# Kernel optimization log

Measured on AMD Instinct MI355X. Metric: run time of the kernel, lower is better.

Reference implementation:

```python
import jax, jax.numpy as jnp
import numpy as np

B, S, D = 16, 512, 13 * 768  # batch, pad_size, (num_layers+1)*hidden
H1, H2 = 1000, 40


def setup_inputs() -> dict:
    key = jax.random.key(0)
    k = jax.random.split(key, 5)
    hidden_states = jax.random.normal(k[0], (B, S, D), dtype=jnp.float32)
    # monotonically increasing subword start indices; 0 == padding slot
    token_starts = jnp.sort(jax.random.randint(k[1], (B, S), 0, S), axis=1).astype(jnp.int64)
    W1 = jax.random.normal(k[2], (D, H1), dtype=jnp.float32) * 0.02
    b1 = jnp.zeros((H1,), dtype=jnp.float32)
    W2 = jax.random.normal(k[3], (H1, H2), dtype=jnp.float32) * 0.02
    b2 = jnp.zeros((H2,), dtype=jnp.float32)
    W3 = jax.random.normal(k[4], (H2, 1), dtype=jnp.float32) * 0.02
    b3 = jnp.zeros((1,), dtype=jnp.float32)
    return {"hidden_states": hidden_states, "token_starts": token_starts,
            "W1": W1, "b1": b1, "W2": W2, "b2": b2, "W3": W3, "b3": b3}


def reference(hidden_states, token_starts, W1, b1, W2, b2, W3, b3):
    # MLP head over concatenated per-layer hidden states: [B,S,D] -> [B,S]
    h = jax.nn.relu(jnp.einsum('bsd,dh->bsh', hidden_states, W1) + b1)
    h = jax.nn.relu(jnp.einsum('bsh,hk->bsk', h, W2) + b2)
    pred_logits = jax.nn.sigmoid(jnp.einsum('bsk,ko->bso', h, W3) + b3)[..., 0]  # [B,S]
    # ragged gather: pred_labels[b,w] = pred_logits[b, token_starts[b,w]] if start != 0 else 0
    gathered = jnp.take_along_axis(pred_logits, token_starts, axis=1)
    pred_labels = jnp.where(token_starts != 0, gathered, jnp.float32(0.0))
    return pred_labels
```

## Files before the change

### kernel.cpp

```cpp
#include <hip/hip_runtime.h>

typedef __bf16 bf16x8 __attribute__((ext_vector_type(8)));
typedef float  f32x4  __attribute__((ext_vector_type(4)));

#define D_DIM 9984
#define H1P   1024
#define M_DIM 8192

__device__ __forceinline__ void gld_lds16(const void* g, void* l) {
  __builtin_amdgcn_global_load_lds((__attribute__((address_space(1))) void*)(g),
                                   (__attribute__((address_space(3))) void*)(l),
                                   16, 0, 0);
}

__global__ __launch_bounds__(256) void k_cvt_a(const float* __restrict__ A,
                                               __bf16* __restrict__ Ab) {
  const size_t t = (size_t)blockIdx.x * 256 + threadIdx.x;
  const float4* p = (const float4*)A + t * 2;
  const float4 a = p[0], b = p[1];
  bf16x8 o;
  o[0] = (__bf16)a.x; o[1] = (__bf16)a.y; o[2] = (__bf16)a.z; o[3] = (__bf16)a.w;
  o[4] = (__bf16)b.x; o[5] = (__bf16)b.y; o[6] = (__bf16)b.z; o[7] = (__bf16)b.w;
  *(bf16x8*)(Ab + t * 8) = o;
}

__global__ __launch_bounds__(256) void k_transpose_w1(const float* __restrict__ W1,
                                                      __bf16* __restrict__ W1T) {
  __shared__ float tile[32][33];
  const int bk = blockIdx.x, bn = blockIdx.y;
  const int tx = threadIdx.x, ty = threadIdx.y;
#pragma unroll
  for (int i = 0; i < 4; ++i) {
    const int kk = bk * 32 + ty + i * 8;
    const int nn = bn * 32 + tx;
    tile[ty + i * 8][tx] = (nn < 1000) ? W1[(size_t)kk * 1000 + nn] : 0.f;
  }
  __syncthreads();
#pragma unroll
  for (int i = 0; i < 4; ++i) {
    const int nn = bn * 32 + ty + i * 8;
    const int kk = bk * 32 + tx;
    W1T[(size_t)nn * D_DIM + kk] = (__bf16)tile[tx][ty + i * 8];
  }
}

__global__ void k_prep_w2(const float* __restrict__ W2, __bf16* __restrict__ W2T) {
  const int idx = blockIdx.x * 256 + threadIdx.x;
  const int j = idx >> 10, k = idx & 1023;
  const float v = (j < 40 && k < 1000) ? W2[k * 40 + j] : 0.f;
  W2T[idx] = (__bf16)v;
}

__global__ __launch_bounds__(256) void k_gemm1b(const __bf16* __restrict__ A,
                                                const __bf16* __restrict__ BT,
                                                const float* __restrict__ b1,
                                                __bf16* __restrict__ C) {
  __shared__ __bf16 As[128 * 32];
  __shared__ __bf16 Bs[128 * 32];
  const int tid  = threadIdx.x;
  const int lane = tid & 63;
  const int wid  = tid >> 6;
  const int tm = blockIdx.x, tn = blockIdx.y;
  const int wm = wid & 1, wn = wid >> 1;

  const int c0 = wid * 2, c1 = c0 + 1;
  const int lr = lane >> 2;
  const int lc = (lane & 3) * 8;
  const __bf16* ag0 = A  + (size_t)(tm * 128 + c0 * 16 + lr) * D_DIM + lc;
  const __bf16* ag1 = A  + (size_t)(tm * 128 + c1 * 16 + lr) * D_DIM + lc;
  const __bf16* bg0 = BT + (size_t)(tn * 128 + c0 * 16 + lr) * D_DIM + lc;
  const __bf16* bg1 = BT + (size_t)(tn * 128 + c1 * 16 + lr) * D_DIM + lc;
  __bf16* al0 = &As[c0 * 16 * 32];
  __bf16* al1 = &As[c1 * 16 * 32];
  __bf16* bl0 = &Bs[c0 * 16 * 32];
  __bf16* bl1 = &Bs[c1 * 16 * 32];

  const int fr = lane & 15;
  const int kq = (lane >> 4) * 8;
  f32x4 acc[4][4] = {};

  for (int i = 0; i < 312; ++i) {
    const size_t k0 = (size_t)i * 32;
    __syncthreads();
    gld_lds16(ag0 + k0, al0);
    gld_lds16(ag1 + k0, al1);
    gld_lds16(bg0 + k0, bl0);
    gld_lds16(bg1 + k0, bl1);
    __syncthreads();
    bf16x8 af[4], bf[4];
#pragma unroll
    for (int mi = 0; mi < 4; ++mi)
      af[mi] = *(const bf16x8*)&As[(wm * 64 + mi * 16 + fr) * 32 + kq];
#pragma unroll
    for (int ni = 0; ni < 4; ++ni)
      bf[ni] = *(const bf16x8*)&Bs[(wn * 64 + ni * 16 + fr) * 32 + kq];
#pragma unroll
    for (int mi = 0; mi < 4; ++mi)
#pragma unroll
      for (int ni = 0; ni < 4; ++ni)
        acc[mi][ni] = __builtin_amdgcn_mfma_f32_16x16x32_bf16(af[mi], bf[ni], acc[mi][ni], 0, 0, 0);
  }

  const int row0 = tm * 128 + wm * 64 + ((lane >> 4) << 2);
  const int col0 = tn * 128 + wn * 64 + fr;
#pragma unroll
  for (int ni = 0; ni < 4; ++ni) {
    const int col = col0 + ni * 16;
    const float bias = (col < 1000) ? b1[col] : 0.f;
#pragma unroll
    for (int mi = 0; mi < 4; ++mi)
#pragma unroll
      for (int r = 0; r < 4; ++r) {
        const float v = acc[mi][ni][r] + bias;
        C[(size_t)(row0 + mi * 16 + r) * H1P + col] = (__bf16)fmaxf(v, 0.f);
      }
  }
}

__global__ __launch_bounds__(256) void k_gemm1(const float* __restrict__ A,
                                               const __bf16* __restrict__ BT,
                                               const float* __restrict__ b1,
                                               __bf16* __restrict__ C) {
  __shared__ __bf16 As[128 * 32];
  __shared__ __bf16 Bs[128 * 32];
  const int tid  = threadIdx.x;
  const int lane = tid & 63;
  const int wid  = tid >> 6;
  const int tm = blockIdx.x, tn = blockIdx.y;
  const int wm = wid & 1, wn = wid >> 1;

  const int arow = tid >> 1;
  const int acol = (tid & 1) * 16;
  const float* ag = A + (size_t)(tm * 128 + arow) * D_DIM + acol;
  __bf16* asw = &As[arow * 32 + acol];

  const int c0 = wid * 2, c1 = wid * 2 + 1;
  const __bf16* bg0 = BT + (size_t)(tn * 128 + c0 * 16 + (lane >> 2)) * D_DIM + (lane & 3) * 8;
  const __bf16* bg1 = BT + (size_t)(tn * 128 + c1 * 16 + (lane >> 2)) * D_DIM + (lane & 3) * 8;
  __bf16* bl0 = &Bs[c0 * 16 * 32];
  __bf16* bl1 = &Bs[c1 * 16 * 32];

  const int fr = lane & 15;
  const int kq = (lane >> 4) * 8;
  f32x4 acc[4][4] = {};

  float4 pa[4];
  {
    const float4* ap = (const float4*)ag;
    pa[0] = ap[0]; pa[1] = ap[1]; pa[2] = ap[2]; pa[3] = ap[3];
  }
  for (int i = 0; i < 312; ++i) {
    const int k0 = i * 32;
    __syncthreads();
    {
      const float* pf = (const float*)pa;
      bf16x8 w0, w1;
#pragma unroll
      for (int j = 0; j < 8; ++j) { w0[j] = (__bf16)pf[j]; w1[j] = (__bf16)pf[j + 8]; }
      *(bf16x8*)asw       = w0;
      *(bf16x8*)(asw + 8) = w1;
    }
    gld_lds16(bg0 + k0, bl0);
    gld_lds16(bg1 + k0, bl1);
    __syncthreads();
    if (i != 311) {
      const float4* ap = (const float4*)(ag + k0 + 32);
      pa[0] = ap[0]; pa[1] = ap[1]; pa[2] = ap[2]; pa[3] = ap[3];
    }
    bf16x8 af[4], bf[4];
#pragma unroll
    for (int mi = 0; mi < 4; ++mi)
      af[mi] = *(const bf16x8*)&As[(wm * 64 + mi * 16 + fr) * 32 + kq];
#pragma unroll
    for (int ni = 0; ni < 4; ++ni)
      bf[ni] = *(const bf16x8*)&Bs[(wn * 64 + ni * 16 + fr) * 32 + kq];
#pragma unroll
    for (int mi = 0; mi < 4; ++mi)
#pragma unroll
      for (int ni = 0; ni < 4; ++ni)
        acc[mi][ni] = __builtin_amdgcn_mfma_f32_16x16x32_bf16(af[mi], bf[ni], acc[mi][ni], 0, 0, 0);
  }
  const int row0 = tm * 128 + wm * 64 + ((lane >> 4) << 2);
  const int col0 = tn * 128 + wn * 64 + fr;
#pragma unroll
  for (int ni = 0; ni < 4; ++ni) {
    const int col = col0 + ni * 16;
    const float bias = (col < 1000) ? b1[col] : 0.f;
#pragma unroll
    for (int mi = 0; mi < 4; ++mi)
#pragma unroll
      for (int r = 0; r < 4; ++r) {
        const float v = acc[mi][ni][r] + bias;
        C[(size_t)(row0 + mi * 16 + r) * H1P + col] = (__bf16)fmaxf(v, 0.f);
      }
  }
}

__global__ __launch_bounds__(256) void k_gemm2l(const __bf16* __restrict__ h1,
                                                const __bf16* __restrict__ W2T,
                                                const float* __restrict__ b2,
                                                const float* __restrict__ W3,
                                                const float* __restrict__ b3,
                                                float* __restrict__ lg) {
  __shared__ __bf16 As[64 * 32];
  __shared__ __bf16 Bs[64 * 32];
  const int tid  = threadIdx.x;
  const int lane = tid & 63;
  const int wid  = tid >> 6;
  const int bm   = blockIdx.x;

  const __bf16* ag = h1  + (size_t)(bm * 64 + wid * 16 + (lane >> 2)) * H1P + (lane & 3) * 8;
  const __bf16* bg = W2T + (size_t)(wid * 16 + (lane >> 2)) * H1P + (lane & 3) * 8;
  __bf16* al = &As[wid * 16 * 32];
  __bf16* bl = &Bs[wid * 16 * 32];

  const int fr = lane & 15;
  const int kq = (lane >> 4) * 8;
  f32x4 acc[4] = {};

  for (int i = 0; i < 32; ++i) {
    const int k0 = i * 32;
    __syncthreads();
    gld_lds16(ag + k0, al);
    gld_lds16(bg + k0, bl);
    __syncthreads();
    const bf16x8 a = *(const bf16x8*)&As[(wid * 16 + fr) * 32 + kq];
#pragma unroll
    for (int ni = 0; ni < 4; ++ni) {
      const bf16x8 b = *(const bf16x8*)&Bs[(ni * 16 + fr) * 32 + kq];
      acc[ni] = __builtin_amdgcn_mfma_f32_16x16x32_bf16(a, b, acc[ni], 0, 0, 0);
    }
  }
  float s[4] = {0.f, 0.f, 0.f, 0.f};
#pragma unroll
  for (int ni = 0; ni < 4; ++ni) {
    const int j = ni * 16 + fr;
    if (j < 40) {
      const float w3 = W3[j], bias = b2[j];
#pragma unroll
      for (int r = 0; r < 4; ++r)
        s[r] += fmaxf(acc[ni][r] + bias, 0.f) * w3;
    }
  }
#pragma unroll
  for (int off = 1; off < 16; off <<= 1)
#pragma unroll
    for (int r = 0; r < 4; ++r)
      s[r] += __shfl_xor(s[r], off, 16);
  if (fr == 0) {
    const int m0 = bm * 64 + wid * 16 + ((lane >> 4) << 2);
    const float b3v = b3[0];
#pragma unroll
    for (int r = 0; r < 4; ++r)
      lg[m0 + r] = 1.f / (1.f + __expf(-(s[r] + b3v)));
  }
}

__global__ void k_gather(const int* __restrict__ ts, const float* __restrict__ lg,
                         float* __restrict__ out) {
  const int t = blockIdx.x * 256 + threadIdx.x;
  const int b = t >> 9;
  const int s = ts[t];
  out[t] = (s > 0 && s < 512) ? lg[(b << 9) + s] : 0.f;
}

extern "C" void kernel_launch(void* const* d_in, const int* in_sizes, int n_in,
                              void* d_out, int out_size, void* d_ws, size_t ws_size,
                              hipStream_t stream) {
  const float* hs = (const float*)d_in[0];
  const int*   ts = (const int*)d_in[1];
  const float* W1 = (const float*)d_in[2];
  const float* b1 = (const float*)d_in[3];
  const float* W2 = (const float*)d_in[4];
  const float* b2 = (const float*)d_in[5];
  const float* W3 = (const float*)d_in[6];
  const float* b3 = (const float*)d_in[7];
  float* out = (float*)d_out;
  char* ws = (char*)d_ws;

  const size_t ABF = 163577856;
  const size_t NEED = ABF + 20447232 + 16777216 + 131072 + 32768;

  if (ws_size >= NEED) {
    __bf16* Ab  = (__bf16*)(ws);
    __bf16* W1T = (__bf16*)(ws + ABF);
    __bf16* h1  = (__bf16*)(ws + ABF + 20447232);
    __bf16* W2T = (__bf16*)(ws + ABF + 20447232 + 16777216);
    float*  lg  = (float*) (ws + ABF + 20447232 + 16777216 + 131072);

    k_cvt_a<<<39936, 256, 0, stream>>>(hs, Ab);
    k_transpose_w1<<<dim3(312, 32), dim3(32, 8), 0, stream>>>(W1, W1T);
    k_prep_w2<<<256, 256, 0, stream>>>(W2, W2T);
    k_gemm1b<<<dim3(64, 8), 256, 0, stream>>>(Ab, W1T, b1, h1);
    k_gemm2l<<<128, 256, 0, stream>>>(h1, W2T, b2, W3, b3, lg);
    k_gather<<<32, 256, 0, stream>>>(ts, lg, out);
  } else {
    __bf16* W1T = (__bf16*)(ws);
    __bf16* h1  = (__bf16*)(ws + 20447232);
    __bf16* W2T = (__bf16*)(ws + 20447232 + 16777216);
    float*  lg  = (float*) (ws + 20447232 + 16777216 + 131072);

    k_transpose_w1<<<dim3(312, 32), dim3(32, 8), 0, stream>>>(W1, W1T);
    k_prep_w2<<<256, 256, 0, stream>>>(W2, W2T);
    k_gemm1<<<dim3(64, 8), 256, 0, stream>>>(hs, W1T, b1, h1);
    k_gemm2l<<<128, 256, 0, stream>>>(h1, W2T, b2, W3, b3, lg);
    k_gather<<<32, 256, 0, stream>>>(ts, lg, out);
  }
}
```

Baseline: 724.6 us.

## Fuse prep kernels and add 4-stage async LDS pipeline to GEMM1

Merges the activation conversion, W1 transpose and W2 prep into one launch, cutting launch gaps. Replaces the GEMM1 main loop, which synchronised twice per K step, with a 4-buffer software pipeline: global-to-LDS loads run three tiles ahead, gated by vmcnt waits and one barrier per step, with raised priority around the MFMAs. GEMM2 gets double-buffered LDS. The pipelined GEMM uses 64KB of LDS per block, which may lower occupancy.

```diff
diff --git a/kernel.cpp b/kernel.cpp
--- a/kernel.cpp
+++ b/kernel.cpp
@@ -5,7 +5,6 @@
 
 #define D_DIM 9984
 #define H1P   1024
-#define M_DIM 8192
 
 __device__ __forceinline__ void gld_lds16(const void* g, void* l) {
   __builtin_amdgcn_global_load_lds((__attribute__((address_space(1))) void*)(g),
@@ -13,50 +12,60 @@
                                    16, 0, 0);
 }
 
-__global__ __launch_bounds__(256) void k_cvt_a(const float* __restrict__ A,
-                                               __bf16* __restrict__ Ab) {
-  const size_t t = (size_t)blockIdx.x * 256 + threadIdx.x;
-  const float4* p = (const float4*)A + t * 2;
-  const float4 a = p[0], b = p[1];
-  bf16x8 o;
-  o[0] = (__bf16)a.x; o[1] = (__bf16)a.y; o[2] = (__bf16)a.z; o[3] = (__bf16)a.w;
-  o[4] = (__bf16)b.x; o[5] = (__bf16)b.y; o[6] = (__bf16)b.z; o[7] = (__bf16)b.w;
-  *(bf16x8*)(Ab + t * 8) = o;
-}
-
-__global__ __launch_bounds__(256) void k_transpose_w1(const float* __restrict__ W1,
-                                                      __bf16* __restrict__ W1T) {
+#define WAITB(N) do {                                              \
+    asm volatile("s_waitcnt vmcnt(" #N ")" ::: "memory");          \
+    __builtin_amdgcn_s_barrier();                                  \
+    __builtin_amdgcn_sched_barrier(0);                             \
+  } while (0)
+
+__global__ __launch_bounds__(256) void k_prep(const float* __restrict__ A,
+                                              __bf16* __restrict__ Ab,
+                                              const float* __restrict__ W1,
+                                              __bf16* __restrict__ W1T,
+                                              const float* __restrict__ W2,
+                                              __bf16* __restrict__ W2T,
+                                              int abase_blocks) {
   __shared__ float tile[32][33];
-  const int bk = blockIdx.x, bn = blockIdx.y;
-  const int tx = threadIdx.x, ty = threadIdx.y;
-#pragma unroll
-  for (int i = 0; i < 4; ++i) {
-    const int kk = bk * 32 + ty + i * 8;
-    const int nn = bn * 32 + tx;
-    tile[ty + i * 8][tx] = (nn < 1000) ? W1[(size_t)kk * 1000 + nn] : 0.f;
-  }
-  __syncthreads();
-#pragma unroll
-  for (int i = 0; i < 4; ++i) {
-    const int nn = bn * 32 + ty + i * 8;
-    const int kk = bk * 32 + tx;
-    W1T[(size_t)nn * D_DIM + kk] = (__bf16)tile[tx][ty + i * 8];
-  }
-}
-
-__global__ void k_prep_w2(const float* __restrict__ W2, __bf16* __restrict__ W2T) {
-  const int idx = blockIdx.x * 256 + threadIdx.x;
-  const int j = idx >> 10, k = idx & 1023;
-  const float v = (j < 40 && k < 1000) ? W2[k * 40 + j] : 0.f;
-  W2T[idx] = (__bf16)v;
-}
-
-__global__ __launch_bounds__(256) void k_gemm1b(const __bf16* __restrict__ A,
+  const int bx  = blockIdx.x;
+  const int tid = threadIdx.x;
+  if (bx < abase_blocks) {
+    const size_t t = (size_t)bx * 256 + tid;
+    const float4* p = (const float4*)A + t * 2;
+    const float4 a = p[0], b = p[1];
+    bf16x8 o;
+    o[0] = (__bf16)a.x; o[1] = (__bf16)a.y; o[2] = (__bf16)a.z; o[3] = (__bf16)a.w;
+    o[4] = (__bf16)b.x; o[5] = (__bf16)b.y; o[6] = (__bf16)b.z; o[7] = (__bf16)b.w;
+    *(bf16x8*)(Ab + t * 8) = o;
+  } else if (bx < abase_blocks + 9984) {
+    const int b = bx - abase_blocks;
+    const int bk = b % 312, bn = b / 312;
+    const int tx = tid & 31, ty = tid >> 5;
+#pragma unroll
+    for (int i = 0; i < 4; ++i) {
+      const int kk = bk * 32 + ty + i * 8;
+      const int nn = bn * 32 + tx;
+      tile[ty + i * 8][tx] = (nn < 1000) ? W1[(size_t)kk * 1000 + nn] : 0.f;
+    }
+    __syncthreads();
+#pragma unroll
+    for (int i = 0; i < 4; ++i) {
+      const int nn = bn * 32 + ty + i * 8;
+      const int kk = bk * 32 + tx;
+      W1T[(size_t)nn * D_DIM + kk] = (__bf16)tile[tx][ty + i * 8];
+    }
+  } else {
+    const int idx = (bx - abase_blocks - 9984) * 256 + tid;
+    const int j = idx >> 10, k = idx & 1023;
+    const float v = (j < 40 && k < 1000) ? W2[k * 40 + j] : 0.f;
+    W2T[idx] = (__bf16)v;
+  }
+}
+
+__global__ __launch_bounds__(256) void k_gemm1p(const __bf16* __restrict__ A,
                                                 const __bf16* __restrict__ BT,
                                                 const float* __restrict__ b1,
                                                 __bf16* __restrict__ C) {
-  __shared__ __bf16 As[128 * 32];
-  __shared__ __bf16 Bs[128 * 32];
+  __shared__ __bf16 lds[4][8192];
   const int tid  = threadIdx.x;
   const int lane = tid & 63;
   const int wid  = tid >> 6;
@@ -70,36 +79,52 @@
   const __bf16* ag1 = A  + (size_t)(tm * 128 + c1 * 16 + lr) * D_DIM + lc;
   const __bf16* bg0 = BT + (size_t)(tn * 128 + c0 * 16 + lr) * D_DIM + lc;
   const __bf16* bg1 = BT + (size_t)(tn * 128 + c1 * 16 + lr) * D_DIM + lc;
-  __bf16* al0 = &As[c0 * 16 * 32];
-  __bf16* al1 = &As[c1 * 16 * 32];
-  __bf16* bl0 = &Bs[c0 * 16 * 32];
-  __bf16* bl1 = &Bs[c1 * 16 * 32];
+  const int ao0 = c0 * 512, ao1 = c1 * 512;
 
   const int fr = lane & 15;
   const int kq = (lane >> 4) * 8;
   f32x4 acc[4][4] = {};
 
-  for (int i = 0; i < 312; ++i) {
-    const size_t k0 = (size_t)i * 32;
-    __syncthreads();
-    gld_lds16(ag0 + k0, al0);
-    gld_lds16(ag1 + k0, al1);
-    gld_lds16(bg0 + k0, bl0);
-    gld_lds16(bg1 + k0, bl1);
-    __syncthreads();
-    bf16x8 af[4], bf[4];
-#pragma unroll
-    for (int mi = 0; mi < 4; ++mi)
-      af[mi] = *(const bf16x8*)&As[(wm * 64 + mi * 16 + fr) * 32 + kq];
-#pragma unroll
-    for (int ni = 0; ni < 4; ++ni)
-      bf[ni] = *(const bf16x8*)&Bs[(wn * 64 + ni * 16 + fr) * 32 + kq];
-#pragma unroll
-    for (int mi = 0; mi < 4; ++mi)
-#pragma unroll
-      for (int ni = 0; ni < 4; ++ni)
-        acc[mi][ni] = __builtin_amdgcn_mfma_f32_16x16x32_bf16(af[mi], bf[ni], acc[mi][ni], 0, 0, 0);
-  }
+#define STAGE(t) do {                                                \
+    __bf16* L_ = &lds[(t) & 3][0];                                   \
+    const size_t k0_ = (size_t)(t) * 32;                             \
+    gld_lds16(ag0 + k0_, L_ + ao0);                                  \
+    gld_lds16(ag1 + k0_, L_ + ao1);                                  \
+    gld_lds16(bg0 + k0_, L_ + 4096 + ao0);                           \
+    gld_lds16(bg1 + k0_, L_ + 4096 + ao1);                           \
+  } while (0)
+
+#define COMPUTE(t) do {                                              \
+    const __bf16* L_ = &lds[(t) & 3][0];                             \
+    bf16x8 af_[4], bf_[4];                                           \
+    _Pragma("unroll")                                                \
+    for (int mi = 0; mi < 4; ++mi)                                   \
+      af_[mi] = *(const bf16x8*)&L_[(wm * 64 + mi * 16 + fr) * 32 + kq]; \
+    _Pragma("unroll")                                                \
+    for (int ni = 0; ni < 4; ++ni)                                   \
+      bf_[ni] = *(const bf16x8*)&L_[4096 + (wn * 64 + ni * 16 + fr) * 32 + kq]; \
+    __builtin_amdgcn_s_setprio(1);                                   \
+    _Pragma("unroll")                                                \
+    for (int mi = 0; mi < 4; ++mi)                                   \
+      _Pragma("unroll")                                              \
+      for (int ni = 0; ni < 4; ++ni)                                 \
+        acc[mi][ni] = __builtin_amdgcn_mfma_f32_16x16x32_bf16(af_[mi], bf_[ni], acc[mi][ni], 0, 0, 0); \
+    __builtin_amdgcn_s_setprio(0);                                   \
+  } while (0)
+
+  STAGE(0); STAGE(1); STAGE(2);
+#pragma unroll 1
+  for (int t = 0; t < 309; ++t) {
+    WAITB(8);
+    STAGE(t + 3);
+    COMPUTE(t);
+  }
+  WAITB(8);  COMPUTE(309);
+  WAITB(4);  COMPUTE(310);
+  WAITB(0);  COMPUTE(311);
+
+#undef STAGE
+#undef COMPUTE
 
   const int row0 = tm * 128 + wm * 64 + ((lane >> 4) << 2);
   const int col0 = tn * 128 + wn * 64 + fr;
@@ -114,6 +139,70 @@
         const float v = acc[mi][ni][r] + bias;
         C[(size_t)(row0 + mi * 16 + r) * H1P + col] = (__bf16)fmaxf(v, 0.f);
       }
+  }
+}
+
+__global__ __launch_bounds__(256) void k_gemm2l(const __bf16* __restrict__ h1,
+                                                const __bf16* __restrict__ W2T,
+                                                const float* __restrict__ b2,
+                                                const float* __restrict__ W3,
+                                                const float* __restrict__ b3,
+                                                float* __restrict__ lg) {
+  __shared__ __align__(16) __bf16 As[2][64 * 32];
+  __shared__ __align__(16) __bf16 Bs[2][64 * 32];
+  const int tid  = threadIdx.x;
+  const int lane = tid & 63;
+  const int wid  = tid >> 6;
+  const int bm   = blockIdx.x;
+
+  const __bf16* ag = h1  + (size_t)(bm * 64 + wid * 16 + (lane >> 2)) * H1P + (lane & 3) * 8;
+  const __bf16* bg = W2T + (size_t)(wid * 16 + (lane >> 2)) * H1P + (lane & 3) * 8;
+  const int wo = wid * 16 * 32;
+
+  const int fr = lane & 15;
+  const int kq = (lane >> 4) * 8;
+  f32x4 acc[4] = {};
+
+  gld_lds16(ag, &As[0][wo]);
+  gld_lds16(bg, &Bs[0][wo]);
+  __syncthreads();
+
+  for (int i = 0; i < 32; ++i) {
+    const int cur = i & 1;
+    if (i < 31) {
+      gld_lds16(ag + (i + 1) * 32, &As[cur ^ 1][wo]);
+      gld_lds16(bg + (i + 1) * 32, &Bs[cur ^ 1][wo]);
+    }
+    const bf16x8 a = *(const bf16x8*)&As[cur][(wid * 16 + fr) * 32 + kq];
+#pragma unroll
+    for (int ni = 0; ni < 4; ++ni) {
+      const bf16x8 b = *(const bf16x8*)&Bs[cur][(ni * 16 + fr) * 32 + kq];
+      acc[ni] = __builtin_amdgcn_mfma_f32_16x16x32_bf16(a, b, acc[ni], 0, 0, 0);
+    }
+    __syncthreads();
+  }
+  float s[4] = {0.f, 0.f, 0.f, 0.f};
+#pragma unroll
+  for (int ni = 0; ni < 4; ++ni) {
+    const int j = ni * 16 + fr;
+    if (j < 40) {
+      const float w3 = W3[j], bias = b2[j];
+#pragma unroll
+      for (int r = 0; r < 4; ++r)
+        s[r] += fmaxf(acc[ni][r] + bias, 0.f) * w3;
+    }
+  }
+#pragma unroll
+  for (int off = 1; off < 16; off <<= 1)
+#pragma unroll
+    for (int r = 0; r < 4; ++r)
+      s[r] += __shfl_xor(s[r], off, 16);
+  if (fr == 0) {
+    const int m0 = bm * 64 + wid * 16 + ((lane >> 4) << 2);
+    const float b3v = b3[0];
+#pragma unroll
+    for (int r = 0; r < 4; ++r)
+      lg[m0 + r] = 1.f / (1.f + __expf(-(s[r] + b3v)));
   }
 }
 
@@ -167,18 +256,18 @@
       const float4* ap = (const float4*)(ag + k0 + 32);
       pa[0] = ap[0]; pa[1] = ap[1]; pa[2] = ap[2]; pa[3] = ap[3];
     }
-    bf16x8 af[4], bf[4];
+    bf16x8 af[4], bfr[4];
 #pragma unroll
     for (int mi = 0; mi < 4; ++mi)
       af[mi] = *(const bf16x8*)&As[(wm * 64 + mi * 16 + fr) * 32 + kq];
 #pragma unroll
     for (int ni = 0; ni < 4; ++ni)
-      bf[ni] = *(const bf16x8*)&Bs[(wn * 64 + ni * 16 + fr) * 32 + kq];
+      bfr[ni] = *(const bf16x8*)&Bs[(wn * 64 + ni * 16 + fr) * 32 + kq];
 #pragma unroll
     for (int mi = 0; mi < 4; ++mi)
 #pragma unroll
       for (int ni = 0; ni < 4; ++ni)
-        acc[mi][ni] = __builtin_amdgcn_mfma_f32_16x16x32_bf16(af[mi], bf[ni], acc[mi][ni], 0, 0, 0);
+        acc[mi][ni] = __builtin_amdgcn_mfma_f32_16x16x32_bf16(af[mi], bfr[ni], acc[mi][ni], 0, 0, 0);
   }
   const int row0 = tm * 128 + wm * 64 + ((lane >> 4) << 2);
   const int col0 = tn * 128 + wn * 64 + fr;
@@ -193,66 +282,6 @@
         const float v = acc[mi][ni][r] + bias;
         C[(size_t)(row0 + mi * 16 + r) * H1P + col] = (__bf16)fmaxf(v, 0.f);
       }
-  }
-}
-
-__global__ __launch_bounds__(256) void k_gemm2l(const __bf16* __restrict__ h1,
-                                                const __bf16* __restrict__ W2T,
-                                                const float* __restrict__ b2,
-                                                const float* __restrict__ W3,
-                                                const float* __restrict__ b3,
-                                                float* __restrict__ lg) {
-  __shared__ __bf16 As[64 * 32];
-  __shared__ __bf16 Bs[64 * 32];
-  const int tid  = threadIdx.x;
-  const int lane = tid & 63;
-  const int wid  = tid >> 6;
-  const int bm   = blockIdx.x;
-
-  const __bf16* ag = h1  + (size_t)(bm * 64 + wid * 16 + (lane >> 2)) * H1P + (lane & 3) * 8;
-  const __bf16* bg = W2T + (size_t)(wid * 16 + (lane >> 2)) * H1P + (lane & 3) * 8;
-  __bf16* al = &As[wid * 16 * 32];
-  __bf16* bl = &Bs[wid * 16 * 32];
-
-  const int fr = lane & 15;
-  const int kq = (lane >> 4) * 8;
-  f32x4 acc[4] = {};
-
-  for (int i = 0; i < 32; ++i) {
-    const int k0 = i * 32;
-    __syncthreads();
-    gld_lds16(ag + k0, al);
-    gld_lds16(bg + k0, bl);
-    __syncthreads();
-    const bf16x8 a = *(const bf16x8*)&As[(wid * 16 + fr) * 32 + kq];
-#pragma unroll
-    for (int ni = 0; ni < 4; ++ni) {
-      const bf16x8 b = *(const bf16x8*)&Bs[(ni * 16 + fr) * 32 + kq];
-      acc[ni] = __builtin_amdgcn_mfma_f32_16x16x32_bf16(a, b, acc[ni], 0, 0, 0);
-    }
-  }
-  float s[4] = {0.f, 0.f, 0.f, 0.f};
-#pragma unroll
-  for (int ni = 0; ni < 4; ++ni) {
-    const int j = ni * 16 + fr;
-    if (j < 40) {
-      const float w3 = W3[j], bias = b2[j];
-#pragma unroll
-      for (int r = 0; r < 4; ++r)
-        s[r] += fmaxf(acc[ni][r] + bias, 0.f) * w3;
-    }
-  }
-#pragma unroll
-  for (int off = 1; off < 16; off <<= 1)
-#pragma unroll
-    for (int r = 0; r < 4; ++r)
-      s[r] += __shfl_xor(s[r], off, 16);
-  if (fr == 0) {
-    const int m0 = bm * 64 + wid * 16 + ((lane >> 4) << 2);
-    const float b3v = b3[0];
-#pragma unroll
-    for (int r = 0; r < 4; ++r)
-      lg[m0 + r] = 1.f / (1.f + __expf(-(s[r] + b3v)));
   }
 }
 
@@ -278,30 +307,28 @@
   float* out = (float*)d_out;
   char* ws = (char*)d_ws;
 
-  const size_t ABF = 163577856;
-  const size_t NEED = ABF + 20447232 + 16777216 + 131072 + 32768;
+  const size_t ABF   = 163577856;
+  const size_t W1TSZ = 20447232;
+  const size_t NEED  = ABF + W1TSZ + 16777216 + 131072 + 32768;
 
   if (ws_size >= NEED) {
     __bf16* Ab  = (__bf16*)(ws);
     __bf16* W1T = (__bf16*)(ws + ABF);
-    __bf16* h1  = (__bf16*)(ws + ABF + 20447232);
-    __bf16* W2T = (__bf16*)(ws + ABF + 20447232 + 16777216);
-    float*  lg  = (float*) (ws + ABF + 20447232 + 16777216 + 131072);
-
-    k_cvt_a<<<39936, 256, 0, stream>>>(hs, Ab);
-    k_transpose_w1<<<dim3(312, 32), dim3(32, 8), 0, stream>>>(W1, W1T);
-    k_prep_w2<<<256, 256, 0, stream>>>(W2, W2T);
-    k_gemm1b<<<dim3(64, 8), 256, 0, stream>>>(Ab, W1T, b1, h1);
+    __bf16* h1  = (__bf16*)(ws + ABF + W1TSZ);
+    __bf16* W2T = (__bf16*)(ws + ABF + W1TSZ + 16777216);
+    float*  lg  = (float*) (ws + ABF + W1TSZ + 16777216 + 131072);
+
+    k_prep<<<39936 + 9984 + 256, 256, 0, stream>>>(hs, Ab, W1, W1T, W2, W2T, 39936);
+    k_gemm1p<<<dim3(64, 8), 256, 0, stream>>>(Ab, W1T, b1, h1);
     k_gemm2l<<<128, 256, 0, stream>>>(h1, W2T, b2, W3, b3, lg);
     k_gather<<<32, 256, 0, stream>>>(ts, lg, out);
   } else {
     __bf16* W1T = (__bf16*)(ws);
-    __bf16* h1  = (__bf16*)(ws + 20447232);
-    __bf16* W2T = (__bf16*)(ws + 20447232 + 16777216);
-    float*  lg  = (float*) (ws + 20447232 + 16777216 + 131072);
-
-    k_transpose_w1<<<dim3(312, 32), dim3(32, 8), 0, stream>>>(W1, W1T);
-    k_prep_w2<<<256, 256, 0, stream>>>(W2, W2T);
+    __bf16* h1  = (__bf16*)(ws + W1TSZ);
+    __bf16* W2T = (__bf16*)(ws + W1TSZ + 16777216);
+    float*  lg  = (float*) (ws + W1TSZ + 16777216 + 131072);
+
+    k_prep<<<9984 + 256, 256, 0, stream>>>(hs, (__bf16*)h1, W1, W1T, W2, W2T, 0);
     k_gemm1<<<dim3(64, 8), 256, 0, stream>>>(hs, W1T, b1, h1);
     k_gemm2l<<<128, 256, 0, stream>>>(h1, W2T, b2, W3, b3, lg);
     k_gather<<<32, 256, 0, stream>>>(ts, lg, out);
```

Result: faster. 706.0 us (-2.6%).
